# Optimization experiments

Hardware: AMD Instinct MI355X
Metric: run time of the kernel (lower is better)

## Reference

```python
import jax, jax.numpy as jnp
import numpy as np
import math

B, LAT, HID, T, NCLS = 128, 128, 256, 1920, 3
EPS = 1e-5


def _ln(x, g, b):
    m = jnp.mean(x, axis=-1, keepdims=True)
    v = jnp.var(x, axis=-1, keepdims=True)
    return (x - m) * jax.lax.rsqrt(v + EPS) * g + b


def _leaky(x):
    return jax.nn.leaky_relu(x, 0.2)


def _lstm_layer(x, Wih, Whh, bih, bhh):
    # x: [T, B, D] time-major; gate order i,f,g,o (PyTorch convention)
    xw = jnp.einsum('tbd,gd->tbg', x, Wih) + bih + bhh  # precompute input projection
    Hd = Whh.shape[1]
    bsz = x.shape[1]

    def step(carry, xg):
        h, c = carry
        gates = xg + h @ Whh.T
        i, f, g, o = jnp.split(gates, 4, axis=-1)
        c = jax.nn.sigmoid(f) * c + jax.nn.sigmoid(i) * jnp.tanh(g)
        h = jax.nn.sigmoid(o) * jnp.tanh(c)
        return (h, c), h

    init = (jnp.zeros((bsz, Hd), x.dtype), jnp.zeros((bsz, Hd), x.dtype))
    _, hs = jax.lax.scan(step, init, xw)
    return hs  # [T, B, H]


def setup_inputs() -> dict:
    key = jax.random.key(0)
    ks = jax.random.split(key, 16)
    s = 0.05
    H2 = HID // 2
    d = {
        'z': jax.random.normal(ks[0], (B, LAT), jnp.float32),
        'labels': jax.random.randint(ks[1], (B,), 0, 4, jnp.int64),
        'emb_W': jax.random.normal(ks[2], (NCLS + 1, HID), jnp.float32) * s,
        'np_W': jax.random.normal(ks[3], (HID, LAT + HID), jnp.float32) * s,
        'np_b': jnp.zeros((HID,), jnp.float32),
        'np_g': jnp.ones((HID,), jnp.float32),
        'np_be': jnp.zeros((HID,), jnp.float32),
        'Wih0': jax.random.normal(ks[4], (4 * HID, 2 * HID), jnp.float32) * s,
        'Whh0': jax.random.normal(ks[5], (4 * HID, HID), jnp.float32) * s,
        'bih0': jnp.zeros((4 * HID,), jnp.float32),
        'bhh0': jnp.zeros((4 * HID,), jnp.float32),
        'Wih1': jax.random.normal(ks[6], (4 * HID, HID), jnp.float32) * s,
        'Whh1': jax.random.normal(ks[7], (4 * HID, HID), jnp.float32) * s,
        'bih1': jnp.zeros((4 * HID,), jnp.float32),
        'bhh1': jnp.zeros((4 * HID,), jnp.float32),
        'oW1': jax.random.normal(ks[8], (H2, HID), jnp.float32) * s,
        'ob1': jnp.zeros((H2,), jnp.float32),
        'og': jnp.ones((H2,), jnp.float32),
        'obe': jnp.zeros((H2,), jnp.float32),
        'oW2': jax.random.normal(ks[9], (3, H2), jnp.float32) * s,
        'ob2': jnp.zeros((3,), jnp.float32),
        'sW1': jax.random.normal(ks[10], (H2, HID), jnp.float32) * s,
        'sb1': jnp.zeros((H2,), jnp.float32),
        'sg': jnp.ones((H2,), jnp.float32),
        'sbe': jnp.zeros((H2,), jnp.float32),
        'sW2': jax.random.normal(ks[11], (1, H2), jnp.float32) * s,
        'sb2': jnp.zeros((1,), jnp.float32),
        'stress_w': jnp.array(1.8, jnp.float32),
        'amu_w': jnp.array([0.15, 0.7, 0.15], jnp.float32),
        'amu_b': jnp.array(-0.3, jnp.float32),
    }
    return d


def reference(z, labels, emb_W, np_W, np_b, np_g, np_be, Wih0, Whh0, bih0, bhh0,
              Wih1, Whh1, bih1, bhh1, oW1, ob1, og, obe, oW2, ob2,
              sW1, sb1, sg, sbe, sW2, sb2, stress_w, amu_w, amu_b):
    bsz = z.shape[0]
    emb = emb_W[labels]                                   # [B, H]
    h = _leaky(_ln(jnp.concatenate([z, emb], axis=1) @ np_W.T + np_b, np_g, np_be))
    # [B, T, 2H]
    sig_in = jnp.concatenate([
        jnp.broadcast_to(h[:, None, :], (bsz, T, HID)),
        jnp.broadcast_to(emb[:, None, :], (bsz, T, HID)),
    ], axis=2)
    x = jnp.transpose(sig_in, (1, 0, 2))                  # time-major [T, B, 2H]
    x = _lstm_layer(x, Wih0, Whh0, bih0, bhh0)
    x = _lstm_layer(x, Wih1, Whh1, bih1, bhh1)
    ch = jnp.transpose(x, (1, 0, 2))                      # [B, T, H]

    # oscillation params per sample (vectorized over batch)
    h_avg = jnp.mean(ch, axis=1)                          # [B, H]
    op = _leaky(_ln(h_avg @ oW1.T + ob1, og, obe)) @ oW2.T + ob2  # [B, 3]
    freq = 0.23 + 0.04 * jnp.tanh(op[:, 0])
    amp = 2.0 + 1.5 * jnp.tanh(op[:, 1])
    phase = math.pi * jax.nn.sigmoid(op[:, 2])
    t = jnp.linspace(0.0, 1.0, T)
    osc = amp[:, None] * jnp.sin(2.0 * math.pi * freq[:, None] * T * t[None, :] + phase[:, None])  # [B, T]

    base = jnp.tanh(_leaky(_ln(ch @ sW1.T + sb1, sg, sbe)) @ sW2.T + sb2)  # [B, T, 1]
    enhanced = 0.6 * base[..., 0] + 0.4 * osc             # [B, T]

    stressed = stress_w * enhanced                        # conv1d k=1, w=1.8
    xp = jnp.pad(enhanced, ((0, 0), (1, 1)))
    smoothed = amu_w[0] * xp[:, :-2] + amu_w[1] * xp[:, 1:-1] + amu_w[2] * xp[:, 2:] + amu_b

    lab = labels[:, None]
    out = jnp.where(lab == 1, enhanced,
          jnp.where(lab == 2, stressed,
          jnp.where(lab == 3, smoothed, jnp.zeros_like(enhanced))))
    return out[..., None]                                  # [B, T, 1]
```

## Files before the change

### kernel.cpp

```cpp
#include <hip/hip_runtime.h>

#define TSTEPS 1920
#define NB 128
#define HIDN 256
#define LATN 128
#define EPSF 1e-5f

typedef __attribute__((ext_vector_type(8))) short bf16x8;
typedef __attribute__((ext_vector_type(4))) float f32x4;

__device__ __forceinline__ unsigned short f2bf(float x) {
    unsigned u = __builtin_bit_cast(unsigned, x);
    unsigned r = (u + 0x7fffu + ((u >> 16) & 1u)) >> 16;
    return (unsigned short)r;
}
__device__ __forceinline__ float bf2f(unsigned short h) {
    unsigned u = ((unsigned)h) << 16;
    return __builtin_bit_cast(float, u);
}
__device__ __forceinline__ float fsig(float x) {
    float e = __expf(-fabsf(x));
    float s = 1.f / (1.f + e);
    return x >= 0.f ? s : 1.f - s;
}
__device__ __forceinline__ float ftanh(float x) {
    float e = __expf(-2.f * fabsf(x));
    float r = (1.f - e) / (1.f + e);
    return x >= 0.f ? r : -r;
}
__device__ __forceinline__ float fleaky(float x) { return x > 0.f ? x : 0.2f * x; }
__device__ __forceinline__ bf16x8 bcast16(uint4 v) { return __builtin_bit_cast(bf16x8, v); }

__device__ __forceinline__ unsigned aload(const unsigned* p) {
    return __hip_atomic_load(p, __ATOMIC_RELAXED, __HIP_MEMORY_SCOPE_AGENT);
}
__device__ __forceinline__ void astore(unsigned* p, unsigned v) {
    __hip_atomic_store(p, v, __ATOMIC_RELAXED, __HIP_MEMORY_SCOPE_AGENT);
}

#define MFMA(a, b, c) __builtin_amdgcn_mfma_f32_16x16x32_bf16((a), (b), (c), 0, 0, 0)

#define FLG(ph, g, s) (((ph) * 8 + (g)) * 8 + (s)) * 32
#define HPLANE(g, layer, buf) (((g) * 2 + (layer)) * 2 + (buf)) * 4096

__global__ void init_sync(unsigned* hbuf, unsigned* flags) {
    int i = blockIdx.x * 256 + threadIdx.x;
    if (i < 131072) hbuf[i] = 0u;
    if (i < 4096) flags[i] = 0u;
}

__global__ void pack_bfrag_sliced(const float* __restrict__ A, const float* __restrict__ Bsrc,
                                  int KA, int KB,
                                  unsigned short* __restrict__ hi, unsigned short* __restrict__ lo) {
    int e = blockIdx.x * 256 + threadIdx.x;
    int K = KA + KB;
    int KT = K >> 5;
    if (e >= 1024 * K) return;
    int j = e & 7;
    int l = (e >> 3) & 63;
    int r = e >> 9;
    int kt = r % KT;
    int r2 = r / KT;
    int v = r2 & 7;
    int w = r2 >> 3;
    int n = (v >> 1) * 256 + 32 * w + 16 * (v & 1) + (l & 15);
    int k = kt * 32 + (l >> 4) * 8 + j;
    float val = (k < KA) ? A[n * KA + k] : Bsrc[n * KB + (k - KA)];
    unsigned short h = f2bf(val);
    hi[e] = h;
    lo[e] = f2bf(val - bf2f(h));
}

__global__ void pack_sw1kj(const float* __restrict__ sW1, unsigned short* __restrict__ out) {
    int e = blockIdx.x * 256 + threadIdx.x;
    if (e >= 256 * 128) return;
    int j = e & 127, k = e >> 7;
    out[e] = f2bf(sW1[j * 256 + k]);
}

__global__ void pack4T(const float* __restrict__ W, int N, int K, float* __restrict__ out) {
    int e = blockIdx.x * 256 + threadIdx.x;
    if (e >= N * K) return;
    int j = e & 3;
    int rest = e >> 2;
    int n = rest % N;
    int k4 = rest / N;
    out[e] = W[n * K + 4 * k4 + j];
}

__global__ void prep_b1(const float* __restrict__ bih1, const float* __restrict__ bhh1,
                        float* __restrict__ b1sum) {
    int i = blockIdx.x * 256 + threadIdx.x;
    if (i < 1024) b1sum[i] = bih1[i] + bhh1[i];
}

__global__ void np_head(const float* __restrict__ z, const int* __restrict__ labels,
                        const float* __restrict__ emb_W, const float* __restrict__ np_W,
                        const float* __restrict__ np_b, const float* __restrict__ np_g,
                        const float* __restrict__ np_be, float* __restrict__ x_const) {
    int b = blockIdx.x;
    int j = threadIdx.x;
    __shared__ float xc[LATN + HIDN];
    __shared__ float red[8];
    int lab = labels[b];
    if (j < LATN) xc[j] = z[b * LATN + j];
    float e = emb_W[lab * HIDN + j];
    xc[LATN + j] = e;
    __syncthreads();
    float d = np_b[j];
    for (int k = 0; k < LATN + HIDN; ++k) d += xc[k] * np_W[j * (LATN + HIDN) + k];
    int lane = j & 63, wv = j >> 6;
    float s = d, s2 = d * d;
    for (int o = 1; o < 64; o <<= 1) { s += __shfl_xor(s, o); s2 += __shfl_xor(s2, o); }
    if (lane == 0) { red[wv] = s; red[4 + wv] = s2; }
    __syncthreads();
    float S = red[0] + red[1] + red[2] + red[3];
    float S2 = red[4] + red[5] + red[6] + red[7];
    float m = S * (1.f / 256.f);
    float var = S2 * (1.f / 256.f) - m * m;
    float h = fleaky((d - m) * rsqrtf(var + EPSF) * np_g[j] + np_be[j]);
    x_const[b * 512 + j] = h;
    x_const[b * 512 + 256 + j] = e;
}

__global__ void __launch_bounds__(1024) xw0_kernel(const float* __restrict__ x_const,
                                                   const float4* __restrict__ Wih0T4,
                                                   const float* __restrict__ bih0,
                                                   const float* __restrict__ bhh0,
                                                   float* __restrict__ xw0) {
    int b = blockIdx.x;
    int g = threadIdx.x;
    __shared__ float xc[512];
    if (g < 512) xc[g] = x_const[b * 512 + g];
    __syncthreads();
    const float4* xc4 = (const float4*)xc;
    float4 acc = {0.f, 0.f, 0.f, 0.f};
#pragma unroll 8
    for (int k4 = 0; k4 < 128; ++k4) {
        float4 w = Wih0T4[k4 * 1024 + g];
        float4 x = xc4[k4];
        acc.x = fmaf(w.x, x.x, acc.x);
        acc.y = fmaf(w.y, x.y, acc.y);
        acc.z = fmaf(w.z, x.z, acc.z);
        acc.w = fmaf(w.w, x.w, acc.w);
    }
    xw0[b * 1024 + g] = bih0[g] + bhh0[g] + ((acc.x + acc.y) + (acc.z + acc.w));
}

__global__ void __launch_bounds__(512, 2) lstm_coop(
    const uint4* __restrict__ whh0h, const uint4* __restrict__ whh0l,
    const uint4* __restrict__ w1h, const uint4* __restrict__ w1l,
    const unsigned short* __restrict__ sw1kj_g, const float* __restrict__ xw0g,
    const float* __restrict__ b1sum, const float* __restrict__ sb1,
    const float* __restrict__ sg, const float* __restrict__ sbe,
    const float* __restrict__ sW2, const float* __restrict__ sb2,
    unsigned* __restrict__ hbuf, unsigned* __restrict__ flags,
    float* __restrict__ base_out, float* __restrict__ hsum_out) {
    extern __shared__ char smem[];
    unsigned short* hhi = (unsigned short*)smem;
    unsigned short* hlo = (unsigned short*)(smem + 16384);
    unsigned short* sw1s = (unsigned short*)(smem + 32768);
    float* gatesL = (float*)(smem + 98304);
    float* ppart = (float*)(smem + 106752);
    char* hhiB = smem;
    char* hloB = smem + 16384;

    const int gidx = blockIdx.x & 7;
    const int W = blockIdx.x >> 3;
    const int g16 = gidx * 16;
    const int tid = threadIdx.x;
    const int l = tid & 63;
    const int v = tid >> 6;
    const int ln16 = l & 15;
    const int kg = l >> 4;

    for (int i = tid; i < 256 * 128; i += 512) sw1s[i] = sw1kj_g[i];
    for (int i = tid; i < 8192; i += 512) { hhi[i] = 0; hlo[i] = 0; }

    uint4 b0h[8], b0l[8];
#pragma unroll
    for (int kt = 0; kt < 8; ++kt) {
        int idx = ((W * 8 + v) * 8 + kt) * 64 + l;
        b0h[kt] = whh0h[idx];
        b0l[kt] = whh0l[idx];
    }
    const uint4* w1hb = w1h + ((W * 8 + v) * 16) * 64 + l;
    const uint4* w1lb = w1l + ((W * 8 + v) * 16) * 64 + l;

    const int row = tid >> 5;
    const int ul = tid & 31;
    const int ug = 32 * W + ul;
    float xwi[4], b1v[4];
#pragma unroll
    for (int gt = 0; gt < 4; ++gt) {
        xwi[gt] = xw0g[(g16 + row) * 1024 + gt * 256 + ug];
        b1v[gt] = b1sum[gt * 256 + ug];
    }
    float c0 = 0.f, c1 = 0.f, hs = 0.f;

    const float sb1a = sb1[l], sb1b = sb1[64 + l];
    const float sga = sg[l], sgb = sg[64 + l];
    const float sbea = sbe[l], sbeb = sbe[64 + l];
    const float sw2a = sW2[l], sw2b = sW2[64 + l];
    const float sb2v = sb2[0];

    unsigned* h0buf[2] = {hbuf + HPLANE(gidx, 0, 0), hbuf + HPLANE(gidx, 0, 1)};
    unsigned* h1buf[2] = {hbuf + HPLANE(gidx, 1, 0), hbuf + HPLANE(gidx, 1, 1)};
    unsigned* fl0 = flags + FLG(0, gidx, W);
    unsigned* fl1 = flags + FLG(1, gidx, W);
    unsigned* fl0base = flags + FLG(0, gidx, 0);
    unsigned* fl1base = flags + FLG(1, gidx, 0);

    const int abase = ln16 * 1024;
    const int aswz = (ln16 & 7) << 4;
    const int kgo = kg * 16;
    const int gcol = (v >> 1) * 32 + (v & 1) * 16 + ln16;
    const int hprow = 2 * W + (v & 1);
    const int hpswz = (hprow & 7) << 4;
    const int kq = v >> 1;

    __syncthreads();

    for (int t = 0; t < TSTEPS; ++t) {
        const int cur = t & 1, prev = cur ^ 1;
        {
            unsigned* src = h1buf[prev];
            for (int i = tid; i < 4096; i += 512) {
                int r_ = i >> 8, u_ = i & 255;
                unsigned val = aload(src + i);
                int off = r_ * 1024 + ((512 + 2 * u_) ^ ((r_ & 7) << 4));
                *(unsigned short*)(hhiB + off) = (unsigned short)(val >> 16);
                *(unsigned short*)(hloB + off) = (unsigned short)(val & 0xffffu);
            }
        }
        __syncthreads();
        {
            f32x4 acc = {0.f, 0.f, 0.f, 0.f};
#pragma unroll
            for (int kt = 0; kt < 8; ++kt) {
                int aoff = abase + ((kt * 64 + kgo) ^ aswz);
                bf16x8 ahi = bcast16(*(const uint4*)(hhiB + aoff));
                bf16x8 alo = bcast16(*(const uint4*)(hloB + aoff));
                bf16x8 bh = bcast16(b0h[kt]);
                bf16x8 bl = bcast16(b0l[kt]);
                acc = MFMA(ahi, bh, acc);
                acc = MFMA(alo, bh, acc);
                acc = MFMA(ahi, bl, acc);
            }
#pragma unroll
            for (int r = 0; r < 4; ++r) gatesL[(kg * 4 + r) * 132 + gcol] = acc[r];
        }
        if (t > 0) {
            float accA = 0.f, accB = 0.f;
            int hb = hprow * 1024;
#pragma unroll 4
            for (int k = kq * 64; k < kq * 64 + 64; ++k) {
                int off = hb + ((512 + 2 * k) ^ hpswz);
                float h = bf2f(*(const unsigned short*)(hhiB + off)) +
                          bf2f(*(const unsigned short*)(hloB + off));
                float wA = bf2f(sw1s[k * 128 + l]);
                float wB = bf2f(sw1s[k * 128 + 64 + l]);
                accA = fmaf(wA, h, accA);
                accB = fmaf(wB, h, accB);
            }
            ppart[(v & 1) * 512 + kq * 128 + l] = accA;
            ppart[(v & 1) * 512 + kq * 128 + 64 + l] = accB;
        }
        __syncthreads();
        {
            float i_ = gatesL[row * 132 + ul] + xwi[0];
            float f_ = gatesL[row * 132 + 32 + ul] + xwi[1];
            float g_ = gatesL[row * 132 + 64 + ul] + xwi[2];
            float o_ = gatesL[row * 132 + 96 + ul] + xwi[3];
            c0 = fsig(f_) * c0 + fsig(i_) * ftanh(g_);
            float h = fsig(o_) * ftanh(c0);
            unsigned short hh = f2bf(h);
            unsigned short ll = f2bf(h - bf2f(hh));
            astore(h0buf[cur] + row * 256 + ug, ((unsigned)hh << 16) | (unsigned)ll);
        }
        asm volatile("s_waitcnt vmcnt(0)" ::: "memory");
        __syncthreads();
        if (tid == 0) astore(fl0, (unsigned)(t + 1));
        {
            unsigned tgt = (unsigned)(t + 1);
            while (true) {
                unsigned val = (l < 8) ? aload(fl0base + l * 32) : tgt;
                if (__all((int)(val >= tgt))) break;
                __builtin_amdgcn_s_sleep(1);
            }
        }
        asm volatile("" ::: "memory");
        {
            unsigned* src = h0buf[cur];
            for (int i = tid; i < 4096; i += 512) {
                int r_ = i >> 8, u_ = i & 255;
                unsigned val = aload(src + i);
                int off = r_ * 1024 + ((2 * u_) ^ ((r_ & 7) << 4));
                *(unsigned short*)(hhiB + off) = (unsigned short)(val >> 16);
                *(unsigned short*)(hloB + off) = (unsigned short)(val & 0xffffu);
            }
        }
        __syncthreads();
        {
            f32x4 acc = {0.f, 0.f, 0.f, 0.f};
#pragma unroll 4
            for (int kt = 0; kt < 16; ++kt) {
                int aoff = abase + ((kt * 64 + kgo) ^ aswz);
                bf16x8 ahi = bcast16(*(const uint4*)(hhiB + aoff));
                bf16x8 alo = bcast16(*(const uint4*)(hloB + aoff));
                bf16x8 bh = bcast16(w1hb[kt * 64]);
                bf16x8 bl = bcast16(w1lb[kt * 64]);
                acc = MFMA(ahi, bh, acc);
                acc = MFMA(alo, bh, acc);
                acc = MFMA(ahi, bl, acc);
            }
#pragma unroll
            for (int r = 0; r < 4; ++r) gatesL[(kg * 4 + r) * 132 + gcol] = acc[r];
        }
        __syncthreads();
        {
            float i_ = gatesL[row * 132 + ul] + b1v[0];
            float f_ = gatesL[row * 132 + 32 + ul] + b1v[1];
            float g_ = gatesL[row * 132 + 64 + ul] + b1v[2];
            float o_ = gatesL[row * 132 + 96 + ul] + b1v[3];
            c1 = fsig(f_) * c1 + fsig(i_) * ftanh(g_);
            float h = fsig(o_) * ftanh(c1);
            hs += h;
            unsigned short hh = f2bf(h);
            unsigned short ll = f2bf(h - bf2f(hh));
            astore(h1buf[cur] + row * 256 + ug, ((unsigned)hh << 16) | (unsigned)ll);
        }
        if (t > 0 && v < 2) {
            float sA = sb1a, sB = sb1b;
#pragma unroll
            for (int q = 0; q < 4; ++q) {
                sA += ppart[v * 512 + q * 128 + l];
                sB += ppart[v * 512 + q * 128 + 64 + l];
            }
            float ssum = sA + sB, ssq = sA * sA + sB * sB;
#pragma unroll
            for (int o = 1; o < 64; o <<= 1) { ssum += __shfl_xor(ssum, o); ssq += __shfl_xor(ssq, o); }
            float m = ssum * (1.f / 128.f);
            float var = ssq * (1.f / 128.f) - m * m;
            float rstd = rsqrtf(var + EPSF);
            float p0 = fleaky((sA - m) * rstd * sga + sbea);
            float p1 = fleaky((sB - m) * rstd * sgb + sbeb);
            float q = p0 * sw2a + p1 * sw2b;
#pragma unroll
            for (int o = 1; o < 64; o <<= 1) q += __shfl_xor(q, o);
            if (l == 0) base_out[(g16 + 2 * W + v) * TSTEPS + (t - 1)] = ftanh(q + sb2v);
        }
        asm volatile("s_waitcnt vmcnt(0)" ::: "memory");
        __syncthreads();
        if (tid == 0) astore(fl1, (unsigned)(t + 1));
        {
            unsigned tgt = (unsigned)(t + 1);
            while (true) {
                unsigned val = (l < 8) ? aload(fl1base + l * 32) : tgt;
                if (__all((int)(val >= tgt))) break;
                __builtin_amdgcn_s_sleep(1);
            }
        }
        asm volatile("" ::: "memory");
    }
    {
        unsigned* src = h1buf[(TSTEPS - 1) & 1];
        for (int i = tid; i < 4096; i += 512) {
            int r_ = i >> 8, u_ = i & 255;
            unsigned val = aload(src + i);
            int off = r_ * 1024 + ((512 + 2 * u_) ^ ((r_ & 7) << 4));
            *(unsigned short*)(hhiB + off) = (unsigned short)(val >> 16);
            *(unsigned short*)(hloB + off) = (unsigned short)(val & 0xffffu);
        }
    }
    __syncthreads();
    {
        float accA = 0.f, accB = 0.f;
        int hb = hprow * 1024;
#pragma unroll 4
        for (int k = kq * 64; k < kq * 64 + 64; ++k) {
            int off = hb + ((512 + 2 * k) ^ hpswz);
            float h = bf2f(*(const unsigned short*)(hhiB + off)) +
                      bf2f(*(const unsigned short*)(hloB + off));
            accA = fmaf(bf2f(sw1s[k * 128 + l]), h, accA);
            accB = fmaf(bf2f(sw1s[k * 128 + 64 + l]), h, accB);
        }
        ppart[(v & 1) * 512 + kq * 128 + l] = accA;
        ppart[(v & 1) * 512 + kq * 128 + 64 + l] = accB;
    }
    __syncthreads();
    if (v < 2) {
        float sA = sb1a, sB = sb1b;
#pragma unroll
        for (int q = 0; q < 4; ++q) {
            sA += ppart[v * 512 + q * 128 + l];
            sB += ppart[v * 512 + q * 128 + 64 + l];
        }
        float ssum = sA + sB, ssq = sA * sA + sB * sB;
#pragma unroll
        for (int o = 1; o < 64; o <<= 1) { ssum += __shfl_xor(ssum, o); ssq += __shfl_xor(ssq, o); }
        float m = ssum * (1.f / 128.f);
        float var = ssq * (1.f / 128.f) - m * m;
        float rstd = rsqrtf(var + EPSF);
        float p0 = fleaky((sA - m) * rstd * sga + sbea);
        float p1 = fleaky((sB - m) * rstd * sgb + sbeb);
        float q = p0 * sw2a + p1 * sw2b;
#pragma unroll
        for (int o = 1; o < 64; o <<= 1) q += __shfl_xor(q, o);
        if (l == 0) base_out[(g16 + 2 * W + v) * TSTEPS + (TSTEPS - 1)] = ftanh(q + sb2v);
    }
    hsum_out[(g16 + row) * HIDN + ug] = hs;
}

__global__ void out_kernel(const float* __restrict__ hsum, const float* __restrict__ oW1,
                           const float* __restrict__ ob1, const float* __restrict__ og,
                           const float* __restrict__ obe, const float* __restrict__ oW2,
                           const float* __restrict__ ob2, const float* __restrict__ base,
                           const int* __restrict__ labels, const float* __restrict__ stress_w,
                           const float* __restrict__ amu_w, const float* __restrict__ amu_b,
                           float* __restrict__ out) {
    int b = blockIdx.x;
    int tid = threadIdx.x;
    int lane = tid & 63, wv = tid >> 6;
    __shared__ float havg[256];
    __shared__ float red[8];
    __shared__ float params[3];
    __shared__ float e_row[TSTEPS];
    havg[tid] = hsum[b * 256 + tid] * (1.f / (float)TSTEPS);
    __syncthreads();
    float d1 = 0.f;
    if (tid < 128) {
        d1 = ob1[tid];
        for (int k = 0; k < 256; ++k) d1 += havg[k] * oW1[tid * 256 + k];
    }
    float s = d1, s2 = d1 * d1;
    for (int o = 1; o < 64; o <<= 1) { s += __shfl_xor(s, o); s2 += __shfl_xor(s2, o); }
    if (lane == 0 && wv < 2) { red[wv] = s; red[2 + wv] = s2; }
    __syncthreads();
    float m = (red[0] + red[1]) * (1.f / 128.f);
    float var = (red[2] + red[3]) * (1.f / 128.f) - m * m;
    float rstd = rsqrtf(var + EPSF);
    float p = 0.f;
    if (tid < 128) p = fleaky((d1 - m) * rstd * og[tid] + obe[tid]);
    float q0 = tid < 128 ? p * oW2[0 * 128 + tid] : 0.f;
    float q1 = tid < 128 ? p * oW2[1 * 128 + tid] : 0.f;
    float q2 = tid < 128 ? p * oW2[2 * 128 + tid] : 0.f;
    for (int o = 1; o < 64; o <<= 1) {
        q0 += __shfl_xor(q0, o); q1 += __shfl_xor(q1, o); q2 += __shfl_xor(q2, o);
    }
    __syncthreads();
    if (lane == 0 && wv < 2) { red[wv] = q0; red[2 + wv] = q1; red[4 + wv] = q2; }
    __syncthreads();
    if (tid == 0) {
        float op0 = red[0] + red[1] + ob2[0];
        float op1 = red[2] + red[3] + ob2[1];
        float op2 = red[4] + red[5] + ob2[2];
        params[0] = 0.23f + 0.04f * ftanh(op0);
        params[1] = 2.0f + 1.5f * ftanh(op1);
        params[2] = 3.14159265358979f * fsig(op2);
    }
    __syncthreads();
    float freq = params[0], amp = params[1], ph = params[2];
    for (int t = tid; t < TSTEPS; t += 256) {
        float x = freq * ((float)TSTEPS * (float)t / (float)(TSTEPS - 1));
        x -= floorf(x);
        float osc = amp * __sinf(6.28318530717958647f * x + ph);
        e_row[t] = 0.6f * base[b * TSTEPS + t] + 0.4f * osc;
    }
    __syncthreads();
    int lab = labels[b];
    float sw = stress_w[0];
    float w0 = amu_w[0], w1 = amu_w[1], w2 = amu_w[2], ab = amu_b[0];
    for (int t = tid; t < TSTEPS; t += 256) {
        float e = e_row[t];
        float r;
        if (lab == 1) r = e;
        else if (lab == 2) r = sw * e;
        else if (lab == 3) {
            float em = t > 0 ? e_row[t - 1] : 0.f;
            float ep = t < TSTEPS - 1 ? e_row[t + 1] : 0.f;
            r = w0 * em + w1 * e + w2 * ep + ab;
        } else r = 0.f;
        out[b * TSTEPS + t] = r;
    }
}

extern "C" void kernel_launch(void* const* d_in, const int* in_sizes, int n_in,
                              void* d_out, int out_size, void* d_ws, size_t ws_size,
                              hipStream_t stream) {
    (void)in_sizes; (void)n_in; (void)out_size; (void)ws_size;
    const float* z      = (const float*)d_in[0];
    const int* labels   = (const int*)d_in[1];
    const float* emb_W  = (const float*)d_in[2];
    const float* np_W   = (const float*)d_in[3];
    const float* np_b   = (const float*)d_in[4];
    const float* np_g   = (const float*)d_in[5];
    const float* np_be  = (const float*)d_in[6];
    const float* Wih0   = (const float*)d_in[7];
    const float* Whh0   = (const float*)d_in[8];
    const float* bih0   = (const float*)d_in[9];
    const float* bhh0   = (const float*)d_in[10];
    const float* Wih1   = (const float*)d_in[11];
    const float* Whh1   = (const float*)d_in[12];
    const float* bih1   = (const float*)d_in[13];
    const float* bhh1   = (const float*)d_in[14];
    const float* oW1    = (const float*)d_in[15];
    const float* ob1    = (const float*)d_in[16];
    const float* og     = (const float*)d_in[17];
    const float* obe    = (const float*)d_in[18];
    const float* oW2    = (const float*)d_in[19];
    const float* ob2    = (const float*)d_in[20];
    const float* sW1    = (const float*)d_in[21];
    const float* sb1    = (const float*)d_in[22];
    const float* sg     = (const float*)d_in[23];
    const float* sbe    = (const float*)d_in[24];
    const float* sW2    = (const float*)d_in[25];
    const float* sb2    = (const float*)d_in[26];
    const float* stressw= (const float*)d_in[27];
    const float* amu_w  = (const float*)d_in[28];
    const float* amu_b  = (const float*)d_in[29];
    float* out = (float*)d_out;

    uint8_t* ws = (uint8_t*)d_ws;
    size_t off = 0;
    unsigned short* whh0h = (unsigned short*)(ws + off); off += (size_t)1024 * 256 * 2;
    unsigned short* whh0l = (unsigned short*)(ws + off); off += (size_t)1024 * 256 * 2;
    unsigned short* w1h   = (unsigned short*)(ws + off); off += (size_t)1024 * 512 * 2;
    unsigned short* w1l   = (unsigned short*)(ws + off); off += (size_t)1024 * 512 * 2;
    unsigned short* sw1kj = (unsigned short*)(ws + off); off += (size_t)256 * 128 * 2;
    float* Wih0T4 = (float*)(ws + off); off += (size_t)1024 * 512 * 4;
    float* x_const= (float*)(ws + off); off += (size_t)NB * 512 * 4;
    float* xw0    = (float*)(ws + off); off += (size_t)NB * 1024 * 4;
    float* b1sum  = (float*)(ws + off); off += (size_t)1024 * 4;
    float* hsum   = (float*)(ws + off); off += (size_t)NB * 256 * 4;
    float* basef  = (float*)(ws + off); off += (size_t)NB * TSTEPS * 4;
    off = (off + 255) & ~(size_t)255;
    unsigned* hbuf = (unsigned*)(ws + off); off += (size_t)131072 * 4;
    unsigned* flags= (unsigned*)(ws + off); off += (size_t)4096 * 4;

    init_sync<<<512, 256, 0, stream>>>(hbuf, flags);
    pack_bfrag_sliced<<<1024, 256, 0, stream>>>(Whh0, nullptr, 256, 0, whh0h, whh0l);
    pack_bfrag_sliced<<<2048, 256, 0, stream>>>(Wih1, Whh1, 256, 256, w1h, w1l);
    pack_sw1kj<<<128, 256, 0, stream>>>(sW1, sw1kj);
    pack4T<<<2048, 256, 0, stream>>>(Wih0, 1024, 512, Wih0T4);
    prep_b1<<<4, 256, 0, stream>>>(bih1, bhh1, b1sum);

    np_head<<<NB, 256, 0, stream>>>(z, labels, emb_W, np_W, np_b, np_g, np_be, x_const);
    xw0_kernel<<<NB, 1024, 0, stream>>>(x_const, (const float4*)Wih0T4, bih0, bhh0, xw0);
    lstm_coop<<<64, 512, 110848, stream>>>((const uint4*)whh0h, (const uint4*)whh0l,
                                           (const uint4*)w1h, (const uint4*)w1l,
                                           sw1kj, xw0, b1sum, sb1, sg, sbe, sW2, sb2,
                                           hbuf, flags, basef, hsum);
    out_kernel<<<NB, 256, 0, stream>>>(hsum, oW1, ob1, og, obe, oW2, ob2, basef, labels,
                                       stressw, amu_w, amu_b, out);
}
```

Baseline: 23.98 ms.

## Process two batch groups per block in persistent LSTM kernel, halving grid

Each persistent LSTM block now handles two 16-row batch groups at once, so the grid goes from 64 to 32 blocks and each block issues twice the MFMA work per weight fragment. The layer-1 hi weights are held in registers, h-state staging uses 64-bit loads, and the sW1 head weights are repacked for vectorized reads. The change also restructures the per-step synchronization so that layer 0 and the head partials overlap with layer 1 inside one step. The intent is to cut synchronization and flag-polling cost per unit of work and improve weight reuse. The cost is more LDS and register pressure and fewer active CUs.

```diff
diff --git a/kernel.cpp b/kernel.cpp
--- a/kernel.cpp
+++ b/kernel.cpp
@@ -18,6 +18,12 @@
     unsigned u = ((unsigned)h) << 16;
     return __builtin_bit_cast(float, u);
 }
+__device__ __forceinline__ float u32lo(unsigned w) {
+    return __builtin_bit_cast(float, w << 16);
+}
+__device__ __forceinline__ float u32hi(unsigned w) {
+    return __builtin_bit_cast(float, w & 0xFFFF0000u);
+}
 __device__ __forceinline__ float fsig(float x) {
     float e = __expf(-fabsf(x));
     float s = 1.f / (1.f + e);
@@ -32,6 +38,9 @@
 __device__ __forceinline__ bf16x8 bcast16(uint4 v) { return __builtin_bit_cast(bf16x8, v); }
 
 __device__ __forceinline__ unsigned aload(const unsigned* p) {
+    return __hip_atomic_load(p, __ATOMIC_RELAXED, __HIP_MEMORY_SCOPE_AGENT);
+}
+__device__ __forceinline__ unsigned long long aload64(const unsigned long long* p) {
     return __hip_atomic_load(p, __ATOMIC_RELAXED, __HIP_MEMORY_SCOPE_AGENT);
 }
 __device__ __forceinline__ void astore(unsigned* p, unsigned v) {
@@ -71,11 +80,11 @@
     lo[e] = f2bf(val - bf2f(h));
 }
 
-__global__ void pack_sw1kj(const float* __restrict__ sW1, unsigned short* __restrict__ out) {
+__global__ void pack_sw1k8(const float* __restrict__ sW1, unsigned short* __restrict__ out) {
     int e = blockIdx.x * 256 + threadIdx.x;
     if (e >= 256 * 128) return;
     int j = e & 127, k = e >> 7;
-    out[e] = f2bf(sW1[j * 256 + k]);
+    out[((k >> 3) * 128 + j) * 8 + (k & 7)] = f2bf(sW1[j * 256 + k]);
 }
 
 __global__ void pack4T(const float* __restrict__ W, int N, int K, float* __restrict__ out) {
@@ -150,32 +159,37 @@
 __global__ void __launch_bounds__(512, 2) lstm_coop(
     const uint4* __restrict__ whh0h, const uint4* __restrict__ whh0l,
     const uint4* __restrict__ w1h, const uint4* __restrict__ w1l,
-    const unsigned short* __restrict__ sw1kj_g, const float* __restrict__ xw0g,
+    const unsigned short* __restrict__ sw1k8_g, const float* __restrict__ xw0g,
     const float* __restrict__ b1sum, const float* __restrict__ sb1,
     const float* __restrict__ sg, const float* __restrict__ sbe,
     const float* __restrict__ sW2, const float* __restrict__ sb2,
     unsigned* __restrict__ hbuf, unsigned* __restrict__ flags,
     float* __restrict__ base_out, float* __restrict__ hsum_out) {
     extern __shared__ char smem[];
-    unsigned short* hhi = (unsigned short*)smem;
-    unsigned short* hlo = (unsigned short*)(smem + 16384);
-    unsigned short* sw1s = (unsigned short*)(smem + 32768);
-    float* gatesL = (float*)(smem + 98304);
-    float* ppart = (float*)(smem + 106752);
-    char* hhiB = smem;
-    char* hloB = smem + 16384;
-
-    const int gidx = blockIdx.x & 7;
-    const int W = blockIdx.x >> 3;
-    const int g16 = gidx * 16;
+    char* pAhi = smem;
+    char* pAlo = smem + 16384;
+    char* pBhi = smem + 32768;
+    char* pBlo = smem + 49152;
+    unsigned short* sw1s = (unsigned short*)(smem + 65536);
+    float* gatesLA = (float*)(smem + 131072);
+    float* gatesLB = (float*)(smem + 139520);
+    float* ppartA = (float*)(smem + 147968);
+    float* ppartB = (float*)(smem + 152064);
+
+    const int W = blockIdx.x & 7;
+    const int q = blockIdx.x >> 3;
+    const int gA = 2 * q, gB = 2 * q + 1;
     const int tid = threadIdx.x;
     const int l = tid & 63;
     const int v = tid >> 6;
     const int ln16 = l & 15;
     const int kg = l >> 4;
 
-    for (int i = tid; i < 256 * 128; i += 512) sw1s[i] = sw1kj_g[i];
-    for (int i = tid; i < 8192; i += 512) { hhi[i] = 0; hlo[i] = 0; }
+    for (int i = tid; i < 256 * 128; i += 512) sw1s[i] = sw1k8_g[i];
+    for (int i = tid; i < 4096; i += 512) {
+        ((unsigned*)pAhi)[i] = 0u; ((unsigned*)pAlo)[i] = 0u;
+        ((unsigned*)pBhi)[i] = 0u; ((unsigned*)pBlo)[i] = 0u;
+    }
 
     uint4 b0h[8], b0l[8];
 #pragma unroll
@@ -184,19 +198,22 @@
         b0h[kt] = whh0h[idx];
         b0l[kt] = whh0l[idx];
     }
-    const uint4* w1hb = w1h + ((W * 8 + v) * 16) * 64 + l;
+    uint4 w1hR[16];
+#pragma unroll
+    for (int kt = 0; kt < 16; ++kt) w1hR[kt] = w1h[((W * 8 + v) * 16 + kt) * 64 + l];
     const uint4* w1lb = w1l + ((W * 8 + v) * 16) * 64 + l;
 
     const int row = tid >> 5;
     const int ul = tid & 31;
     const int ug = 32 * W + ul;
-    float xwi[4], b1v[4];
+    float xwiA[4], xwiB[4], b1v[4];
 #pragma unroll
     for (int gt = 0; gt < 4; ++gt) {
-        xwi[gt] = xw0g[(g16 + row) * 1024 + gt * 256 + ug];
+        xwiA[gt] = xw0g[(gA * 16 + row) * 1024 + gt * 256 + ug];
+        xwiB[gt] = xw0g[(gB * 16 + row) * 1024 + gt * 256 + ug];
         b1v[gt] = b1sum[gt * 256 + ug];
     }
-    float c0 = 0.f, c1 = 0.f, hs = 0.f;
+    float c0A = 0.f, c0B = 0.f, c1A = 0.f, c1B = 0.f, hsA = 0.f, hsB = 0.f;
 
     const float sb1a = sb1[l], sb1b = sb1[64 + l];
     const float sga = sg[l], sgb = sg[64 + l];
@@ -204,12 +221,14 @@
     const float sw2a = sW2[l], sw2b = sW2[64 + l];
     const float sb2v = sb2[0];
 
-    unsigned* h0buf[2] = {hbuf + HPLANE(gidx, 0, 0), hbuf + HPLANE(gidx, 0, 1)};
-    unsigned* h1buf[2] = {hbuf + HPLANE(gidx, 1, 0), hbuf + HPLANE(gidx, 1, 1)};
-    unsigned* fl0 = flags + FLG(0, gidx, W);
-    unsigned* fl1 = flags + FLG(1, gidx, W);
-    unsigned* fl0base = flags + FLG(0, gidx, 0);
-    unsigned* fl1base = flags + FLG(1, gidx, 0);
+    unsigned* h0A[2] = {hbuf + HPLANE(gA, 0, 0), hbuf + HPLANE(gA, 0, 1)};
+    unsigned* h1A[2] = {hbuf + HPLANE(gA, 1, 0), hbuf + HPLANE(gA, 1, 1)};
+    unsigned* h0B[2] = {hbuf + HPLANE(gB, 0, 0), hbuf + HPLANE(gB, 0, 1)};
+    unsigned* h1B[2] = {hbuf + HPLANE(gB, 1, 0), hbuf + HPLANE(gB, 1, 1)};
+    unsigned* fl0 = flags + FLG(0, q, W);
+    unsigned* fl1 = flags + FLG(1, q, W);
+    unsigned* fl0base = flags + FLG(0, q, 0);
+    unsigned* fl1base = flags + FLG(1, q, 0);
 
     const int abase = ln16 * 1024;
     const int aswz = (ln16 & 7) << 4;
@@ -218,198 +237,241 @@
     const int hprow = 2 * W + (v & 1);
     const int hpswz = (hprow & 7) << 4;
     const int kq = v >> 1;
+    const int rpar = v & 1;
+
+#define STAGE(srcA, srcB, baseByte)                                              \
+    {                                                                            \
+        _Pragma("unroll")                                                        \
+        for (int it = 0; it < 4; ++it) {                                         \
+            int i2 = tid + 512 * it;                                             \
+            int r_ = i2 >> 7, u2 = i2 & 127;                                     \
+            int off = r_ * 1024 + (((baseByte) + 4 * u2) ^ ((r_ & 7) << 4));     \
+            unsigned long long vA = aload64(                                     \
+                (const unsigned long long*)(srcA) + r_ * 128 + u2);              \
+            unsigned a0 = (unsigned)vA, a1 = (unsigned)(vA >> 32);               \
+            *(unsigned*)(pAhi + off) = (a0 >> 16) | (a1 & 0xffff0000u);          \
+            *(unsigned*)(pAlo + off) = (a0 & 0xffffu) | (a1 << 16);              \
+            unsigned long long vB = aload64(                                     \
+                (const unsigned long long*)(srcB) + r_ * 128 + u2);              \
+            unsigned e0 = (unsigned)vB, e1 = (unsigned)(vB >> 32);               \
+            *(unsigned*)(pBhi + off) = (e0 >> 16) | (e1 & 0xffff0000u);          \
+            *(unsigned*)(pBlo + off) = (e0 & 0xffffu) | (e1 << 16);              \
+        }                                                                        \
+    }
+
+#define HEADPART                                                                 \
+    {                                                                            \
+        float pAa = 0.f, pAb = 0.f, pBa = 0.f, pBb = 0.f;                        \
+        int hb = hprow * 1024;                                                   \
+        _Pragma("unroll")                                                        \
+        for (int kc = 0; kc < 8; ++kc) {                                         \
+            int kb = kq * 64 + kc * 8;                                           \
+            int poff = hb + ((512 + 2 * kb) ^ hpswz);                            \
+            uint4 hiA = *(const uint4*)(pAhi + poff);                            \
+            uint4 loA = *(const uint4*)(pAlo + poff);                            \
+            uint4 hiB = *(const uint4*)(pBhi + poff);                            \
+            uint4 loB = *(const uint4*)(pBlo + poff);                            \
+            int idx8 = kq * 8 + kc;                                              \
+            uint4 wa4 = *(const uint4*)&sw1s[(idx8 * 128 + l) * 8];              \
+            uint4 wb4 = *(const uint4*)&sw1s[(idx8 * 128 + 64 + l) * 8];         \
+            _Pragma("unroll")                                                    \
+            for (int q_ = 0; q_ < 4; ++q_) {                                     \
+                unsigned hwA = ((const unsigned*)&hiA)[q_];                      \
+                unsigned lwA = ((const unsigned*)&loA)[q_];                      \
+                float heA = u32lo(hwA) + u32lo(lwA);                             \
+                float hoA = u32hi(hwA) + u32hi(lwA);                             \
+                unsigned hwB = ((const unsigned*)&hiB)[q_];                      \
+                unsigned lwB = ((const unsigned*)&loB)[q_];                      \
+                float heB = u32lo(hwB) + u32lo(lwB);                             \
+                float hoB = u32hi(hwB) + u32hi(lwB);                             \
+                unsigned wa = ((const unsigned*)&wa4)[q_];                       \
+                unsigned wb = ((const unsigned*)&wb4)[q_];                       \
+                pAa = fmaf(u32lo(wa), heA, pAa); pAa = fmaf(u32hi(wa), hoA, pAa);\
+                pAb = fmaf(u32lo(wb), heA, pAb); pAb = fmaf(u32hi(wb), hoA, pAb);\
+                pBa = fmaf(u32lo(wa), heB, pBa); pBa = fmaf(u32hi(wa), hoB, pBa);\
+                pBb = fmaf(u32lo(wb), heB, pBb); pBb = fmaf(u32hi(wb), hoB, pBb);\
+            }                                                                    \
+        }                                                                        \
+        ppartA[rpar * 512 + kq * 128 + l] = pAa;                                 \
+        ppartA[rpar * 512 + kq * 128 + 64 + l] = pAb;                            \
+        ppartB[rpar * 512 + kq * 128 + l] = pBa;                                 \
+        ppartB[rpar * 512 + kq * 128 + 64 + l] = pBb;                            \
+    }
+
+#define HEADFIN(tout)                                                            \
+    if (v < 4) {                                                                 \
+        const float* pp = (v >> 1) ? ppartB : ppartA;                            \
+        int rp = v & 1;                                                          \
+        float sA = sb1a, sB = sb1b;                                              \
+        _Pragma("unroll")                                                        \
+        for (int q_ = 0; q_ < 4; ++q_) {                                         \
+            sA += pp[rp * 512 + q_ * 128 + l];                                   \
+            sB += pp[rp * 512 + q_ * 128 + 64 + l];                              \
+        }                                                                        \
+        float ssum = sA + sB, ssq = sA * sA + sB * sB;                           \
+        _Pragma("unroll")                                                        \
+        for (int o = 1; o < 64; o <<= 1) {                                       \
+            ssum += __shfl_xor(ssum, o); ssq += __shfl_xor(ssq, o);              \
+        }                                                                        \
+        float m = ssum * (1.f / 128.f);                                          \
+        float var = ssq * (1.f / 128.f) - m * m;                                 \
+        float rstd = rsqrtf(var + EPSF);                                         \
+        float p0 = fleaky((sA - m) * rstd * sga + sbea);                         \
+        float p1 = fleaky((sB - m) * rstd * sgb + sbeb);                         \
+        float qd = p0 * sw2a + p1 * sw2b;                                        \
+        _Pragma("unroll")                                                        \
+        for (int o = 1; o < 64; o <<= 1) qd += __shfl_xor(qd, o);                \
+        int grow = ((v >> 1) ? gB : gA) * 16 + 2 * W + rp;                       \
+        if (l == 0) base_out[grow * TSTEPS + (tout)] = ftanh(qd + sb2v);         \
+    }
+
+#define WAITF(basep, tgtv)                                                       \
+    {                                                                            \
+        unsigned tgt = (unsigned)(tgtv);                                         \
+        while (true) {                                                           \
+            unsigned val = (l < 8) ? aload((basep) + l * 32) : tgt;              \
+            if (__all((int)(val >= tgt))) break;                                 \
+            __builtin_amdgcn_s_sleep(1);                                         \
+        }                                                                        \
+    }                                                                            \
+    asm volatile("" ::: "memory");
 
     __syncthreads();
 
     for (int t = 0; t < TSTEPS; ++t) {
         const int cur = t & 1, prev = cur ^ 1;
+        WAITF(fl1base, t);
+        STAGE(h1A[prev], h1B[prev], 512);
+        __syncthreads();
+        uint4 lb[8];
+#pragma unroll
+        for (int kt = 0; kt < 8; ++kt) lb[kt] = w1lb[(8 + kt) * 64];
         {
-            unsigned* src = h1buf[prev];
-            for (int i = tid; i < 4096; i += 512) {
-                int r_ = i >> 8, u_ = i & 255;
-                unsigned val = aload(src + i);
-                int off = r_ * 1024 + ((512 + 2 * u_) ^ ((r_ & 7) << 4));
-                *(unsigned short*)(hhiB + off) = (unsigned short)(val >> 16);
-                *(unsigned short*)(hloB + off) = (unsigned short)(val & 0xffffu);
+            f32x4 aA = {0.f, 0.f, 0.f, 0.f}, aB = {0.f, 0.f, 0.f, 0.f};
+#pragma unroll
+            for (int kt = 0; kt < 8; ++kt) {
+                int aoff = abase + ((kt * 64 + kgo) ^ aswz);
+                bf16x8 ahiA = bcast16(*(const uint4*)(pAhi + aoff));
+                bf16x8 aloA = bcast16(*(const uint4*)(pAlo + aoff));
+                bf16x8 ahiB = bcast16(*(const uint4*)(pBhi + aoff));
+                bf16x8 aloB = bcast16(*(const uint4*)(pBlo + aoff));
+                bf16x8 bh = bcast16(b0h[kt]);
+                bf16x8 bl = bcast16(b0l[kt]);
+                aA = MFMA(ahiA, bh, aA); aA = MFMA(aloA, bh, aA); aA = MFMA(ahiA, bl, aA);
+                aB = MFMA(ahiB, bh, aB); aB = MFMA(aloB, bh, aB); aB = MFMA(ahiB, bl, aB);
+            }
+#pragma unroll
+            for (int r = 0; r < 4; ++r) {
+                gatesLA[(kg * 4 + r) * 132 + gcol] = aA[r];
+                gatesLB[(kg * 4 + r) * 132 + gcol] = aB[r];
+            }
+        }
+        f32x4 acc1A = {0.f, 0.f, 0.f, 0.f}, acc1B = {0.f, 0.f, 0.f, 0.f};
+#pragma unroll
+        for (int kt = 8; kt < 16; ++kt) {
+            int aoff = abase + ((kt * 64 + kgo) ^ aswz);
+            bf16x8 ahiA = bcast16(*(const uint4*)(pAhi + aoff));
+            bf16x8 aloA = bcast16(*(const uint4*)(pAlo + aoff));
+            bf16x8 ahiB = bcast16(*(const uint4*)(pBhi + aoff));
+            bf16x8 aloB = bcast16(*(const uint4*)(pBlo + aoff));
+            bf16x8 bh = bcast16(w1hR[kt]);
+            bf16x8 bl = bcast16(lb[kt - 8]);
+            acc1A = MFMA(ahiA, bh, acc1A); acc1A = MFMA(aloA, bh, acc1A); acc1A = MFMA(ahiA, bl, acc1A);
+            acc1B = MFMA(ahiB, bh, acc1B); acc1B = MFMA(aloB, bh, acc1B); acc1B = MFMA(ahiB, bl, acc1B);
+        }
+        HEADPART;
+        __syncthreads();
+        {
+            float i_ = gatesLA[row * 132 + ul] + xwiA[0];
+            float f_ = gatesLA[row * 132 + 32 + ul] + xwiA[1];
+            float g_ = gatesLA[row * 132 + 64 + ul] + xwiA[2];
+            float o_ = gatesLA[row * 132 + 96 + ul] + xwiA[3];
+            c0A = fsig(f_) * c0A + fsig(i_) * ftanh(g_);
+            float h = fsig(o_) * ftanh(c0A);
+            unsigned short hh = f2bf(h);
+            unsigned short ll = f2bf(h - bf2f(hh));
+            astore(h0A[cur] + row * 256 + ug, ((unsigned)hh << 16) | (unsigned)ll);
+            i_ = gatesLB[row * 132 + ul] + xwiB[0];
+            f_ = gatesLB[row * 132 + 32 + ul] + xwiB[1];
+            g_ = gatesLB[row * 132 + 64 + ul] + xwiB[2];
+            o_ = gatesLB[row * 132 + 96 + ul] + xwiB[3];
+            c0B = fsig(f_) * c0B + fsig(i_) * ftanh(g_);
+            h = fsig(o_) * ftanh(c0B);
+            hh = f2bf(h);
+            ll = f2bf(h - bf2f(hh));
+            astore(h0B[cur] + row * 256 + ug, ((unsigned)hh << 16) | (unsigned)ll);
+        }
+        asm volatile("s_waitcnt vmcnt(0)" ::: "memory");
+        __syncthreads();
+        if (tid == 0) astore(fl0, (unsigned)(t + 1));
+        uint4 la[8];
+#pragma unroll
+        for (int kt = 0; kt < 8; ++kt) la[kt] = w1lb[kt * 64];
+        if (t > 0) HEADFIN(t - 1);
+        WAITF(fl0base, t + 1);
+        STAGE(h0A[cur], h0B[cur], 0);
+        __syncthreads();
+        {
+#pragma unroll
+            for (int kt = 0; kt < 8; ++kt) {
+                int aoff = abase + ((kt * 64 + kgo) ^ aswz);
+                bf16x8 ahiA = bcast16(*(const uint4*)(pAhi + aoff));
+                bf16x8 aloA = bcast16(*(const uint4*)(pAlo + aoff));
+                bf16x8 ahiB = bcast16(*(const uint4*)(pBhi + aoff));
+                bf16x8 aloB = bcast16(*(const uint4*)(pBlo + aoff));
+                bf16x8 bh = bcast16(w1hR[kt]);
+                bf16x8 bl = bcast16(la[kt]);
+                acc1A = MFMA(ahiA, bh, acc1A); acc1A = MFMA(aloA, bh, acc1A); acc1A = MFMA(ahiA, bl, acc1A);
+                acc1B = MFMA(ahiB, bh, acc1B); acc1B = MFMA(aloB, bh, acc1B); acc1B = MFMA(ahiB, bl, acc1B);
+            }
+#pragma unroll
+            for (int r = 0; r < 4; ++r) {
+                gatesLA[(kg * 4 + r) * 132 + gcol] = acc1A[r];
+                gatesLB[(kg * 4 + r) * 132 + gcol] = acc1B[r];
             }
         }
         __syncthreads();
         {
-            f32x4 acc = {0.f, 0.f, 0.f, 0.f};
-#pragma unroll
-            for (int kt = 0; kt < 8; ++kt) {
-                int aoff = abase + ((kt * 64 + kgo) ^ aswz);
-                bf16x8 ahi = bcast16(*(const uint4*)(hhiB + aoff));
-                bf16x8 alo = bcast16(*(const uint4*)(hloB + aoff));
-                bf16x8 bh = bcast16(b0h[kt]);
-                bf16x8 bl = bcast16(b0l[kt]);
-                acc = MFMA(ahi, bh, acc);
-                acc = MFMA(alo, bh, acc);
-                acc = MFMA(ahi, bl, acc);
-            }
-#pragma unroll
-            for (int r = 0; r < 4; ++r) gatesL[(kg * 4 + r) * 132 + gcol] = acc[r];
-        }
-        if (t > 0) {
-            float accA = 0.f, accB = 0.f;
-            int hb = hprow * 1024;
-#pragma unroll 4
-            for (int k = kq * 64; k < kq * 64 + 64; ++k) {
-                int off = hb + ((512 + 2 * k) ^ hpswz);
-                float h = bf2f(*(const unsigned short*)(hhiB + off)) +
-                          bf2f(*(const unsigned short*)(hloB + off));
-                float wA = bf2f(sw1s[k * 128 + l]);
-                float wB = bf2f(sw1s[k * 128 + 64 + l]);
-                accA = fmaf(wA, h, accA);
-                accB = fmaf(wB, h, accB);
-            }
-            ppart[(v & 1) * 512 + kq * 128 + l] = accA;
-            ppart[(v & 1) * 512 + kq * 128 + 64 + l] = accB;
-        }
-        __syncthreads();
-        {
-            float i_ = gatesL[row * 132 + ul] + xwi[0];
-            float f_ = gatesL[row * 132 + 32 + ul] + xwi[1];
-            float g_ = gatesL[row * 132 + 64 + ul] + xwi[2];
-            float o_ = gatesL[row * 132 + 96 + ul] + xwi[3];
-            c0 = fsig(f_) * c0 + fsig(i_) * ftanh(g_);
-            float h = fsig(o_) * ftanh(c0);
+            float i_ = gatesLA[row * 132 + ul] + b1v[0];
+            float f_ = gatesLA[row * 132 + 32 + ul] + b1v[1];
+            float g_ = gatesLA[row * 132 + 64 + ul] + b1v[2];
+            float o_ = gatesLA[row * 132 + 96 + ul] + b1v[3];
+            c1A = fsig(f_) * c1A + fsig(i_) * ftanh(g_);
+            float h = fsig(o_) * ftanh(c1A);
+            hsA += h;
             unsigned short hh = f2bf(h);
             unsigned short ll = f2bf(h - bf2f(hh));
-            astore(h0buf[cur] + row * 256 + ug, ((unsigned)hh << 16) | (unsigned)ll);
-        }
-        asm volatile("s_waitcnt vmcnt(0)" ::: "memory");
-        __syncthreads();
-        if (tid == 0) astore(fl0, (unsigned)(t + 1));
-        {
-            unsigned tgt = (unsigned)(t + 1);
-            while (true) {
-                unsigned val = (l < 8) ? aload(fl0base + l * 32) : tgt;
-                if (__all((int)(val >= tgt))) break;
-                __builtin_amdgcn_s_sleep(1);
-            }
-        }
-        asm volatile("" ::: "memory");
-        {
-            unsigned* src = h0buf[cur];
-            for (int i = tid; i < 4096; i += 512) {
-                int r_ = i >> 8, u_ = i & 255;
-                unsigned val = aload(src + i);
-                int off = r_ * 1024 + ((2 * u_) ^ ((r_ & 7) << 4));
-                *(unsigned short*)(hhiB + off) = (unsigned short)(val >> 16);
-                *(unsigned short*)(hloB + off) = (unsigned short)(val & 0xffffu);
-            }
-        }
-        __syncthreads();
-        {
-            f32x4 acc = {0.f, 0.f, 0.f, 0.f};
-#pragma unroll 4
-            for (int kt = 0; kt < 16; ++kt) {
-                int aoff = abase + ((kt * 64 + kgo) ^ aswz);
-                bf16x8 ahi = bcast16(*(const uint4*)(hhiB + aoff));
-                bf16x8 alo = bcast16(*(const uint4*)(hloB + aoff));
-                bf16x8 bh = bcast16(w1hb[kt * 64]);
-                bf16x8 bl = bcast16(w1lb[kt * 64]);
-                acc = MFMA(ahi, bh, acc);
-                acc = MFMA(alo, bh, acc);
-                acc = MFMA(ahi, bl, acc);
-            }
-#pragma unroll
-            for (int r = 0; r < 4; ++r) gatesL[(kg * 4 + r) * 132 + gcol] = acc[r];
-        }
-        __syncthreads();
-        {
-            float i_ = gatesL[row * 132 + ul] + b1v[0];
-            float f_ = gatesL[row * 132 + 32 + ul] + b1v[1];
-            float g_ = gatesL[row * 132 + 64 + ul] + b1v[2];
-            float o_ = gatesL[row * 132 + 96 + ul] + b1v[3];
-            c1 = fsig(f_) * c1 + fsig(i_) * ftanh(g_);
-            float h = fsig(o_) * ftanh(c1);
-            hs += h;
-            unsigned short hh = f2bf(h);
-            unsigned short ll = f2bf(h - bf2f(hh));
-            astore(h1buf[cur] + row * 256 + ug, ((unsigned)hh << 16) | (unsigned)ll);
-        }
-        if (t > 0 && v < 2) {
-            float sA = sb1a, sB = sb1b;
-#pragma unroll
-            for (int q = 0; q < 4; ++q) {
-                sA += ppart[v * 512 + q * 128 + l];
-                sB += ppart[v * 512 + q * 128 + 64 + l];
-            }
-            float ssum = sA + sB, ssq = sA * sA + sB * sB;
-#pragma unroll
-            for (int o = 1; o < 64; o <<= 1) { ssum += __shfl_xor(ssum, o); ssq += __shfl_xor(ssq, o); }
-            float m = ssum * (1.f / 128.f);
-            float var = ssq * (1.f / 128.f) - m * m;
-            float rstd = rsqrtf(var + EPSF);
-            float p0 = fleaky((sA - m) * rstd * sga + sbea);
-            float p1 = fleaky((sB - m) * rstd * sgb + sbeb);
-            float q = p0 * sw2a + p1 * sw2b;
-#pragma unroll
-            for (int o = 1; o < 64; o <<= 1) q += __shfl_xor(q, o);
-            if (l == 0) base_out[(g16 + 2 * W + v) * TSTEPS + (t - 1)] = ftanh(q + sb2v);
+            astore(h1A[cur] + row * 256 + ug, ((unsigned)hh << 16) | (unsigned)ll);
+            i_ = gatesLB[row * 132 + ul] + b1v[0];
+            f_ = gatesLB[row * 132 + 32 + ul] + b1v[1];
+            g_ = gatesLB[row * 132 + 64 + ul] + b1v[2];
+            o_ = gatesLB[row * 132 + 96 + ul] + b1v[3];
+            c1B = fsig(f_) * c1B + fsig(i_) * ftanh(g_);
+            h = fsig(o_) * ftanh(c1B);
+            hsB += h;
+            hh = f2bf(h);
+            ll = f2bf(h - bf2f(hh));
+            astore(h1B[cur] + row * 256 + ug, ((unsigned)hh << 16) | (unsigned)ll);
         }
         asm volatile("s_waitcnt vmcnt(0)" ::: "memory");
         __syncthreads();
         if (tid == 0) astore(fl1, (unsigned)(t + 1));
-        {
-            unsigned tgt = (unsigned)(t + 1);
-            while (true) {
-                unsigned val = (l < 8) ? aload(fl1base + l * 32) : tgt;
-                if (__all((int)(val >= tgt))) break;
-                __builtin_amdgcn_s_sleep(1);
-            }
-        }
-        asm volatile("" ::: "memory");
-    }
+    }
+    WAITF(fl1base, TSTEPS);
     {
-        unsigned* src = h1buf[(TSTEPS - 1) & 1];
-        for (int i = tid; i < 4096; i += 512) {
-            int r_ = i >> 8, u_ = i & 255;
-            unsigned val = aload(src + i);
-            int off = r_ * 1024 + ((512 + 2 * u_) ^ ((r_ & 7) << 4));
-            *(unsigned short*)(hhiB + off) = (unsigned short)(val >> 16);
-            *(unsigned short*)(hloB + off) = (unsigned short)(val & 0xffffu);
-        }
-    }
-    __syncthreads();
-    {
-        float accA = 0.f, accB = 0.f;
-        int hb = hprow * 1024;
-#pragma unroll 4
-        for (int k = kq * 64; k < kq * 64 + 64; ++k) {
-            int off = hb + ((512 + 2 * k) ^ hpswz);
-            float h = bf2f(*(const unsigned short*)(hhiB + off)) +
-                      bf2f(*(const unsigned short*)(hloB + off));
-            accA = fmaf(bf2f(sw1s[k * 128 + l]), h, accA);
-            accB = fmaf(bf2f(sw1s[k * 128 + 64 + l]), h, accB);
-        }
-        ppart[(v & 1) * 512 + kq * 128 + l] = accA;
-        ppart[(v & 1) * 512 + kq * 128 + 64 + l] = accB;
-    }
-    __syncthreads();
-    if (v < 2) {
-        float sA = sb1a, sB = sb1b;
-#pragma unroll
-        for (int q = 0; q < 4; ++q) {
-            sA += ppart[v * 512 + q * 128 + l];
-            sB += ppart[v * 512 + q * 128 + 64 + l];
-        }
-        float ssum = sA + sB, ssq = sA * sA + sB * sB;
-#pragma unroll
-        for (int o = 1; o < 64; o <<= 1) { ssum += __shfl_xor(ssum, o); ssq += __shfl_xor(ssq, o); }
-        float m = ssum * (1.f / 128.f);
-        float var = ssq * (1.f / 128.f) - m * m;
-        float rstd = rsqrtf(var + EPSF);
-        float p0 = fleaky((sA - m) * rstd * sga + sbea);
-        float p1 = fleaky((sB - m) * rstd * sgb + sbeb);
-        float q = p0 * sw2a + p1 * sw2b;
-#pragma unroll
-        for (int o = 1; o < 64; o <<= 1) q += __shfl_xor(q, o);
-        if (l == 0) base_out[(g16 + 2 * W + v) * TSTEPS + (TSTEPS - 1)] = ftanh(q + sb2v);
-    }
-    hsum_out[(g16 + row) * HIDN + ug] = hs;
+        const int prev = (TSTEPS - 1) & 1;
+        STAGE(h1A[prev], h1B[prev], 512);
+    }
+    __syncthreads();
+    HEADPART;
+    __syncthreads();
+    HEADFIN(TSTEPS - 1);
+    hsum_out[(gA * 16 + row) * HIDN + ug] = hsA;
+    hsum_out[(gB * 16 + row) * HIDN + ug] = hsB;
+#undef STAGE
+#undef HEADPART
+#undef HEADFIN
+#undef WAITF
 }
 
 __global__ void out_kernel(const float* __restrict__ hsum, const float* __restrict__ oW1,
@@ -527,7 +589,7 @@
     unsigned short* whh0l = (unsigned short*)(ws + off); off += (size_t)1024 * 256 * 2;
     unsigned short* w1h   = (unsigned short*)(ws + off); off += (size_t)1024 * 512 * 2;
     unsigned short* w1l   = (unsigned short*)(ws + off); off += (size_t)1024 * 512 * 2;
-    unsigned short* sw1kj = (unsigned short*)(ws + off); off += (size_t)256 * 128 * 2;
+    unsigned short* sw1k8 = (unsigned short*)(ws + off); off += (size_t)256 * 128 * 2;
     float* Wih0T4 = (float*)(ws + off); off += (size_t)1024 * 512 * 4;
     float* x_const= (float*)(ws + off); off += (size_t)NB * 512 * 4;
     float* xw0    = (float*)(ws + off); off += (size_t)NB * 1024 * 4;
@@ -541,15 +603,15 @@
     init_sync<<<512, 256, 0, stream>>>(hbuf, flags);
     pack_bfrag_sliced<<<1024, 256, 0, stream>>>(Whh0, nullptr, 256, 0, whh0h, whh0l);
     pack_bfrag_sliced<<<2048, 256, 0, stream>>>(Wih1, Whh1, 256, 256, w1h, w1l);
-    pack_sw1kj<<<128, 256, 0, stream>>>(sW1, sw1kj);
+    pack_sw1k8<<<128, 256, 0, stream>>>(sW1, sw1k8);
     pack4T<<<2048, 256, 0, stream>>>(Wih0, 1024, 512, Wih0T4);
     prep_b1<<<4, 256, 0, stream>>>(bih1, bhh1, b1sum);
 
     np_head<<<NB, 256, 0, stream>>>(z, labels, emb_W, np_W, np_b, np_g, np_be, x_const);
     xw0_kernel<<<NB, 1024, 0, stream>>>(x_const, (const float4*)Wih0T4, bih0, bhh0, xw0);
-    lstm_coop<<<64, 512, 110848, stream>>>((const uint4*)whh0h, (const uint4*)whh0l,
+    lstm_coop<<<32, 512, 156160, stream>>>((const uint4*)whh0h, (const uint4*)whh0l,
                                            (const uint4*)w1h, (const uint4*)w1l,
-                                           sw1kj, xw0, b1sum, sb1, sg, sbe, sW2, sb2,
+                                           sw1k8, xw0, b1sum, sb1, sg, sbe, sW2, sb2,
                                            hbuf, flags, basef, hsum);
     out_kernel<<<NB, 256, 0, stream>>>(hsum, oW1, ob1, og, obe, oW2, ob2, basef, labels,
                                        stressw, amu_w, amu_b, out);
```

Result: slower. 43.05 ms (+79.5%).
